# Kernel tuning notes

Measured on AMD Instinct MI355X. Metric: run time of the kernel, lower is better.

The kernel has to match this reference:

```python
import jax, jax.numpy as jnp
import numpy as np

N, E = 2048, 6144
DV_IN, DV_OUT = 128, 64
DE_IN, DE_OUT = 16, 16


def setup_inputs() -> dict:
    key = jax.random.key(0)
    ks = jax.random.split(key, 11)
    return {
        "H_v": jax.random.normal(ks[0], (N, DV_IN), jnp.float32),
        "H_e": jax.random.normal(ks[1], (E, DE_IN), jnp.float32),
        "adj_v": jax.random.uniform(ks[2], (N, N), jnp.float32),
        "adj_e": jax.random.uniform(ks[3], (E, E), jnp.float32),
        "T": jax.random.normal(ks[4], (N, E), jnp.float32),
        "W_v": jax.random.normal(ks[5], (DV_IN, DV_OUT), jnp.float32) * (1.0 / np.sqrt(DV_OUT)),
        "b_v": jax.random.normal(ks[6], (DV_OUT,), jnp.float32) * 0.01,
        "p_v": jax.random.normal(ks[7], (1, DE_IN), jnp.float32),
        "W_e": jax.random.normal(ks[8], (DE_IN, DE_OUT), jnp.float32) * (1.0 / np.sqrt(DE_OUT)),
        "b_e": jax.random.normal(ks[9], (DE_OUT,), jnp.float32) * 0.01,
        "p_e": jax.random.normal(ks[10], (1, DV_OUT), jnp.float32),
    }


def reference(H_v, H_e, adj_v, adj_e, T, W_v, b_v, p_v, W_e, b_e, p_e):
    n, e = T.shape
    # ---- node layer (AlternateConvolution, node_layer=True) ----
    d_e = (H_e @ p_v.T)[:, 0]                      # [E] per-edge diag values
    mult1 = (T * d_e[None, :]) @ T.T               # T @ diag(d_e) @ T^T -> [N,N]
    idx_n = jnp.arange(n)
    M1 = mult1.at[idx_n, idx_n].set(1.0)           # eye*1 + (1-eye)*multiplier
    adjusted_Av = M1 * adj_v
    Hv_out = adjusted_Av @ (H_v @ W_v) + b_v       # [N, DV_OUT]
    # ---- edge layer (AlternateConvolution, node_layer=False) ----
    d_v = (Hv_out @ p_e.T)[:, 0]                   # [N] per-node diag values
    mult2 = (T.T * d_v[None, :]) @ T               # T^T @ diag(d_v) @ T -> [E,E]
    idx_e = jnp.arange(e)
    M2 = mult2.at[idx_e, idx_e].set(1.0)
    adjusted_Ae = M2 * adj_e
    norm_Ae = adjusted_Ae / (adjusted_Ae.max(axis=0, keepdims=True) + 1e-10)
    He_out = norm_Ae @ (H_e @ W_e) + b_e           # [E, DE_OUT]
    return Hv_out, He_out
```

## Files before the change

### kernel.cpp

```cpp
#include <hip/hip_runtime.h>

typedef unsigned short u16;
typedef unsigned int u32;
typedef __bf16 bf16x8 __attribute__((ext_vector_type(8)));
typedef float f32x4 __attribute__((ext_vector_type(4)));

#define NN 2048
#define NE 6144
#define DVIN 128
#define DVOUT 64
#define DEIN 16
#define DEOUT 16

__device__ __forceinline__ u16 f2b(float f) {
  __bf16 b = (__bf16)f;
  return __builtin_bit_cast(u16, b);
}

__device__ __forceinline__ void async16(const void* g, void* l) {
  __builtin_amdgcn_global_load_lds(
      (const __attribute__((address_space(1))) void*)g,
      (__attribute__((address_space(3))) void*)l, 16, 0, 0);
}

__device__ __forceinline__ bf16x8 load8(const u16* p) {
  union { uint4 u; bf16x8 b; } w;
  w.u = *(const uint4*)p;
  return w.b;
}


__global__ __launch_bounds__(256) void k_de(const float* __restrict__ He,
                                            const float* __restrict__ pv,
                                            float* __restrict__ de) {
  int j = blockIdx.x * 256 + threadIdx.x;
  float s = 0.f;
#pragma unroll
  for (int k = 0; k < DEIN; k++) s += He[j * DEIN + k] * pv[k];
  de[j] = s;
}

__global__ __launch_bounds__(256) void k_tb(const float* __restrict__ T,
                                            const float* __restrict__ de,
                                            u16* __restrict__ Tb,
                                            u16* __restrict__ Tbs) {
  size_t idx = (size_t)blockIdx.x * 256 + threadIdx.x;
  size_t f = idx * 8;
  float4 v0 = *(const float4*)(T + f);
  float4 v1 = *(const float4*)(T + f + 4);
  int col = (int)(f % (size_t)NE);
  float4 d0 = *(const float4*)(de + col);
  float4 d1 = *(const float4*)(de + col + 4);
  float v[8] = {v0.x, v0.y, v0.z, v0.w, v1.x, v1.y, v1.z, v1.w};
  float d[8] = {d0.x, d0.y, d0.z, d0.w, d1.x, d1.y, d1.z, d1.w};
  union { u16 s[8]; uint4 u; } a, b;
#pragma unroll
  for (int j = 0; j < 8; j++) { a.s[j] = f2b(v[j]); b.s[j] = f2b(v[j] * d[j]); }
  *(uint4*)(Tb + f) = a.u;
  *(uint4*)(Tbs + f) = b.u;
}

__global__ __launch_bounds__(256) void k_x(const float* __restrict__ Hv,
                                           const float* __restrict__ Wv,
                                           u16* __restrict__ Xt) {
  int i = blockIdx.x * 256 + threadIdx.x;
  int d = blockIdx.y;
  float s = 0.f;
#pragma unroll 8
  for (int k = 0; k < DVIN; k++) s += Hv[i * DVIN + k] * Wv[k * DVOUT + d];
  Xt[(size_t)d * NN + i] = f2b(s);
}

__global__ __launch_bounds__(256) void k_dv(const float* __restrict__ HvOut,
                                            const float* __restrict__ pe,
                                            float* __restrict__ dv) {
  int i = blockIdx.x * 256 + threadIdx.x;
  float s = 0.f;
#pragma unroll
  for (int c = 0; c < DVOUT; c++) s += HvOut[i * DVOUT + c] * pe[c];
  dv[i] = s;
}

__global__ __launch_bounds__(256) void k_tt(const float* __restrict__ T,
                                            const float* __restrict__ dv,
                                            u16* __restrict__ Tt,
                                            u16* __restrict__ Tts) {
  __shared__ float tile[32][33];
  int tx = threadIdx.x, ty = threadIdx.y;
  int bx = blockIdx.x, by = blockIdx.y;
  int col = bx * 32 + tx;
#pragma unroll
  for (int r = 0; r < 4; r++) {
    int row = by * 32 + ty + r * 8;
    tile[ty + r * 8][tx] = T[(size_t)row * NE + col];
  }
  __syncthreads();
  int ocol = by * 32 + tx;
  float dvv = dv[ocol];
#pragma unroll
  for (int r = 0; r < 4; r++) {
    int orow = bx * 32 + ty + r * 8;
    float v = tile[tx][ty + r * 8];
    Tt[(size_t)orow * NN + ocol] = f2b(v);
    Tts[(size_t)orow * NN + ocol] = f2b(v * dvv);
  }
}

__global__ __launch_bounds__(256) void k_zt(const float* __restrict__ He,
                                            const float* __restrict__ We,
                                            const u32* __restrict__ colmax,
                                            u16* __restrict__ Ztb) {
  int b = blockIdx.x * 256 + threadIdx.x;
  float h[16];
  const float4* hp = (const float4*)(He + (size_t)b * DEIN);
#pragma unroll
  for (int q = 0; q < 4; q++) {
    float4 t = hp[q];
    h[q * 4 + 0] = t.x; h[q * 4 + 1] = t.y; h[q * 4 + 2] = t.z; h[q * 4 + 3] = t.w;
  }
  float inv = 1.0f / (__uint_as_float(colmax[b]) + 1e-10f);
#pragma unroll
  for (int d = 0; d < DEOUT; d++) {
    float s = 0.f;
#pragma unroll
    for (int k = 0; k < DEIN; k++) s += h[k] * We[k * DEOUT + d];
    Ztb[(size_t)d * NE + b] = f2b(s * inv);
  }
}

#define BM 128
#define BN 128
#define BK 64

template <int EPI>
__global__ __launch_bounds__(256) void gemm_bt(const u16* __restrict__ A,
                                               const u16* __restrict__ B,
                                               const float* __restrict__ adj,
                                               u16* __restrict__ C,
                                               u32* __restrict__ colmax,
                                               int M, int N, int K) {
  __shared__ u16 As[BM * BK];
  __shared__ u16 Bs[BN * BK];
  __shared__ u32 cmaxLds[BN];

  const int t = threadIdx.x;
  const int bm0 = blockIdx.y * BM, bn0 = blockIdx.x * BN;
  const int wave = t >> 6, lane = t & 63;
  const int lr = lane & 15, kg = lane >> 4;
  const int wm = (wave >> 1) * 64, wn = (wave & 1) * 64;

  if (EPI == 2 && t < BN) cmaxLds[t] = 0u;

  f32x4 acc[4][4];
#pragma unroll
  for (int i = 0; i < 4; i++)
#pragma unroll
    for (int j = 0; j < 4; j++) acc[i][j] = (f32x4){0.f, 0.f, 0.f, 0.f};

  const int arow = t >> 3;
  const int acolsw = (((t & 7) ^ (arow & 7)) * 8);
  const u16* Ag = A + (size_t)(bm0 + arow) * K + acolsw;
  const u16* Bg = B + (size_t)(bn0 + arow) * K + acolsw;
  u16* Al = &As[t * 8];
  u16* Bl = &Bs[t * 8];

  for (int k0 = 0; k0 < K; k0 += BK) {
    __syncthreads();
#pragma unroll
    for (int r = 0; r < 4; r++) {
      async16(Ag + (size_t)(r * 32) * K + k0, Al + r * 32 * BK);
      async16(Bg + (size_t)(r * 32) * K + k0, Bl + r * 32 * BK);
    }
    __syncthreads();
#pragma unroll
    for (int kk = 0; kk < BK; kk += 32) {
      bf16x8 af[4], bf[4];
#pragma unroll
      for (int mi = 0; mi < 4; mi++) {
        int row = wm + mi * 16 + lr;
        int c = (kk >> 3) + kg;
        af[mi] = load8(&As[row * BK + ((c ^ (row & 7)) << 3)]);
      }
#pragma unroll
      for (int ni = 0; ni < 4; ni++) {
        int row = wn + ni * 16 + lr;
        int c = (kk >> 3) + kg;
        bf[ni] = load8(&Bs[row * BK + ((c ^ (row & 7)) << 3)]);
      }
#pragma unroll
      for (int mi = 0; mi < 4; mi++)
#pragma unroll
        for (int ni = 0; ni < 4; ni++)
          acc[mi][ni] = __builtin_amdgcn_mfma_f32_16x16x32_bf16(
              af[mi], bf[ni], acc[mi][ni], 0, 0, 0);
    }
  }

#pragma unroll
  for (int ni = 0; ni < 4; ni++) {
    const int cj = bn0 + wn + ni * 16 + lr;
    float cm = 0.f;
#pragma unroll
    for (int mi = 0; mi < 4; mi++) {
#pragma unroll
      for (int r = 0; r < 4; r++) {
        const int ci = bm0 + wm + mi * 16 + kg * 4 + r;
        float v = acc[mi][ni][r];
        if (ci == cj) v = 1.0f;
        v *= adj[(size_t)ci * N + cj];
        C[(size_t)ci * N + cj] = f2b(v);
        if (EPI == 2) cm = fmaxf(cm, v);
      }
    }
    if (EPI == 2)
      atomicMax(&cmaxLds[wn + ni * 16 + lr], __float_as_uint(cm));
  }
  if (EPI == 2) {
    __syncthreads();
    if (t < BN) atomicMax(&colmax[bn0 + t], cmaxLds[t]);
  }
}


__global__ __launch_bounds__(256) void k_hv(const u16* __restrict__ A1,
                                            const u16* __restrict__ Xt,
                                            const float* __restrict__ bv,
                                            float* __restrict__ out) {
  __shared__ float red[4 * 1024];
  const int t = threadIdx.x, wave = t >> 6, lane = t & 63;
  const int lr = lane & 15, kg = lane >> 4;
  const int m0 = blockIdx.x * 16;
  const int K = NN;
  f32x4 acc[4];
#pragma unroll
  for (int i = 0; i < 4; i++) acc[i] = (f32x4){0.f, 0.f, 0.f, 0.f};
  const int kbeg = wave * (K / 4), kend = kbeg + (K / 4);
  for (int k = kbeg; k < kend; k += 32) {
    bf16x8 af = load8(&A1[(size_t)(m0 + lr) * K + k + kg * 8]);
#pragma unroll
    for (int ni = 0; ni < 4; ni++) {
      bf16x8 bfr = load8(&Xt[(size_t)(ni * 16 + lr) * K + k + kg * 8]);
      acc[ni] = __builtin_amdgcn_mfma_f32_16x16x32_bf16(af, bfr, acc[ni], 0, 0, 0);
    }
  }
#pragma unroll
  for (int ni = 0; ni < 4; ni++)
#pragma unroll
    for (int r = 0; r < 4; r++)
      red[wave * 1024 + (kg * 4 + r) * 64 + ni * 16 + lr] = acc[ni][r];
  __syncthreads();
#pragma unroll
  for (int q = 0; q < 4; q++) {
    int e = t + 256 * q;
    int row = e >> 6, col = e & 63;
    float v = red[e] + red[1024 + e] + red[2048 + e] + red[3072 + e] + bv[col];
    out[(size_t)(m0 + row) * DVOUT + col] = v;
  }
}

__global__ __launch_bounds__(256) void k_he(const u16* __restrict__ adjE,
                                            const u16* __restrict__ Ztb,
                                            const float* __restrict__ be,
                                            float* __restrict__ out) {
  __shared__ float red[4 * 256];
  const int t = threadIdx.x, wave = t >> 6, lane = t & 63;
  const int lr = lane & 15, kg = lane >> 4;
  const int m0 = blockIdx.x * 16;
  const int K = NE;
  f32x4 acc = (f32x4){0.f, 0.f, 0.f, 0.f};
  const int kbeg = wave * (K / 4), kend = kbeg + (K / 4);
  for (int k = kbeg; k < kend; k += 32) {
    bf16x8 af = load8(&adjE[(size_t)(m0 + lr) * K + k + kg * 8]);
    bf16x8 bfr = load8(&Ztb[(size_t)lr * K + k + kg * 8]);
    acc = __builtin_amdgcn_mfma_f32_16x16x32_bf16(af, bfr, acc, 0, 0, 0);
  }
#pragma unroll
  for (int r = 0; r < 4; r++)
    red[wave * 256 + (kg * 4 + r) * 16 + lr] = acc[r];
  __syncthreads();
  {
    int row = t >> 4, col = t & 15;
    float v = red[t] + red[256 + t] + red[512 + t] + red[768 + t] + be[col];
    out[(size_t)(m0 + row) * DEOUT + col] = v;
  }
}

extern "C" void kernel_launch(void* const* d_in, const int* in_sizes, int n_in,
                              void* d_out, int out_size, void* d_ws, size_t ws_size,
                              hipStream_t stream) {
  const float* H_v = (const float*)d_in[0];
  const float* H_e = (const float*)d_in[1];
  const float* adj_v = (const float*)d_in[2];
  const float* adj_e = (const float*)d_in[3];
  const float* T = (const float*)d_in[4];
  const float* W_v = (const float*)d_in[5];
  const float* b_v = (const float*)d_in[6];
  const float* p_v = (const float*)d_in[7];
  const float* W_e = (const float*)d_in[8];
  const float* b_e = (const float*)d_in[9];
  const float* p_e = (const float*)d_in[10];
  float* outHv = (float*)d_out;
  float* outHe = (float*)d_out + NN * DVOUT;

  char* ws = (char*)d_ws;
  u16* Tb   = (u16*)(ws + 0);
  u16* Tbs  = (u16*)(ws + 25165824);
  u16* Tt   = (u16*)(ws + 50331648);
  u16* Tts  = (u16*)(ws + 75497472);
  u16* adjE = (u16*)(ws + 100663296);
  u16* A1   = (u16*)(ws + 176160768);
  u16* Xt   = (u16*)(ws + 184549376);
  u16* Ztb  = (u16*)(ws + 184811520);
  float* de = (float*)(ws + 185008128);
  float* dv = (float*)(ws + 185032704);
  u32* cmax = (u32*)(ws + 185040896);

  k_de<<<NE / 256, 256, 0, stream>>>(H_e, p_v, de);
  k_tb<<<(NN * (size_t)NE) / 8 / 256, 256, 0, stream>>>(T, de, Tb, Tbs);
  k_x<<<dim3(NN / 256, DVOUT), 256, 0, stream>>>(H_v, W_v, Xt);
  gemm_bt<1><<<dim3(NN / BN, NN / BM), 256, 0, stream>>>(
      Tbs, Tb, adj_v, A1, nullptr, NN, NN, NE);
  k_hv<<<NN / 16, 256, 0, stream>>>(A1, Xt, b_v, outHv);
  k_dv<<<NN / 256, 256, 0, stream>>>(outHv, p_e, dv);
  k_tt<<<dim3(NE / 32, NN / 32), dim3(32, 8), 0, stream>>>(T, dv, Tt, Tts);
  hipMemsetAsync(cmax, 0, NE * sizeof(u32), stream);
  gemm_bt<2><<<dim3(NE / BN, NE / BM), 256, 0, stream>>>(
      Tts, Tt, adj_e, adjE, cmax, NE, NE, NN);
  k_zt<<<NE / 256, 256, 0, stream>>>(H_e, W_e, cmax, Ztb);
  k_he<<<NE / 16, 256, 0, stream>>>(adjE, Ztb, b_e, outHe);
}
```

Before: 643.6 us.

## Exploit symmetry of T·diag·Tᵀ products and split-K the node gemm

Both multiplier matrices are symmetric, so the gemms now compute only upper-triangular tiles and mirror the result through LDS into the transposed tile. The edge gemm writes both tiles and updates column maxima for both. The node gemm also adds a 4-way split-K into fp32 partials, summed by a new combine kernel that applies the diagonal and adjacency mask. This roughly halves the MFMA work, at the cost of extra partial-buffer traffic, an extra launch, and idle blocks below the diagonal.

```diff
diff --git a/kernel.cpp b/kernel.cpp
--- a/kernel.cpp
+++ b/kernel.cpp
@@ -12,9 +12,18 @@
 #define DEIN 16
 #define DEOUT 16
 
+#define BM 128
+#define BN 128
+#define BK 64
+#define MS 132
+
 __device__ __forceinline__ u16 f2b(float f) {
   __bf16 b = (__bf16)f;
   return __builtin_bit_cast(u16, b);
+}
+
+__device__ __forceinline__ float b2f(u16 u) {
+  return __uint_as_float(((u32)u) << 16);
 }
 
 __device__ __forceinline__ void async16(const void* g, void* l) {
@@ -128,34 +137,17 @@
   }
 }
 
-#define BM 128
-#define BN 128
-#define BK 64
-
-template <int EPI>
-__global__ __launch_bounds__(256) void gemm_bt(const u16* __restrict__ A,
-                                               const u16* __restrict__ B,
-                                               const float* __restrict__ adj,
-                                               u16* __restrict__ C,
-                                               u32* __restrict__ colmax,
-                                               int M, int N, int K) {
-  __shared__ u16 As[BM * BK];
-  __shared__ u16 Bs[BN * BK];
-  __shared__ u32 cmaxLds[BN];
-
+__device__ __forceinline__ void tile_loop(const u16* __restrict__ A,
+                                          const u16* __restrict__ B,
+                                          int bm0, int bn0, int K,
+                                          int kbeg, int kend,
+                                          u16* As, u16* Bs,
+                                          f32x4 (&acc)[4][4]) {
   const int t = threadIdx.x;
-  const int bm0 = blockIdx.y * BM, bn0 = blockIdx.x * BN;
-  const int wave = t >> 6, lane = t & 63;
+  const int lane = t & 63;
   const int lr = lane & 15, kg = lane >> 4;
+  const int wave = t >> 6;
   const int wm = (wave >> 1) * 64, wn = (wave & 1) * 64;
-
-  if (EPI == 2 && t < BN) cmaxLds[t] = 0u;
-
-  f32x4 acc[4][4];
-#pragma unroll
-  for (int i = 0; i < 4; i++)
-#pragma unroll
-    for (int j = 0; j < 4; j++) acc[i][j] = (f32x4){0.f, 0.f, 0.f, 0.f};
 
   const int arow = t >> 3;
   const int acolsw = (((t & 7) ^ (arow & 7)) * 8);
@@ -164,7 +156,7 @@
   u16* Al = &As[t * 8];
   u16* Bl = &Bs[t * 8];
 
-  for (int k0 = 0; k0 < K; k0 += BK) {
+  for (int k0 = kbeg; k0 < kend; k0 += BK) {
     __syncthreads();
 #pragma unroll
     for (int r = 0; r < 4; r++) {
@@ -195,29 +187,180 @@
               af[mi], bf[ni], acc[mi][ni], 0, 0, 0);
     }
   }
-
+}
+
+__global__ __launch_bounds__(256) void gemm_sym1(const u16* __restrict__ A,
+                                                 const u16* __restrict__ B,
+                                                 float* __restrict__ P) {
+  const int bi = blockIdx.y, bj = blockIdx.x;
+  if (bj < bi) return;
+  __shared__ u16 As[BM * BK];
+  __shared__ u16 Bs[BN * BK];
+  const int bm0 = bi * BM, bn0 = bj * BN;
+  const int K = NE, kc = NE / 4;
+  f32x4 acc[4][4];
+#pragma unroll
+  for (int i = 0; i < 4; i++)
+#pragma unroll
+    for (int j = 0; j < 4; j++) acc[i][j] = (f32x4){0.f, 0.f, 0.f, 0.f};
+
+  tile_loop(A, B, bm0, bn0, K, blockIdx.z * kc, (blockIdx.z + 1) * kc, As, Bs, acc);
+
+  const int t = threadIdx.x, lane = t & 63, lr = lane & 15, kg = lane >> 4;
+  const int wave = t >> 6, wm = (wave >> 1) * 64, wn = (wave & 1) * 64;
+  float* Pz = P + (size_t)blockIdx.z * NN * NN;
 #pragma unroll
   for (int ni = 0; ni < 4; ni++) {
     const int cj = bn0 + wn + ni * 16 + lr;
-    float cm = 0.f;
-#pragma unroll
-    for (int mi = 0; mi < 4; mi++) {
+#pragma unroll
+    for (int mi = 0; mi < 4; mi++)
 #pragma unroll
       for (int r = 0; r < 4; r++) {
         const int ci = bm0 + wm + mi * 16 + kg * 4 + r;
+        Pz[(size_t)ci * NN + cj] = acc[mi][ni][r];
+      }
+  }
+}
+
+__global__ __launch_bounds__(256) void k_comb(const float* __restrict__ P,
+                                              const float* __restrict__ adj,
+                                              u16* __restrict__ A1) {
+  const int bi = blockIdx.y, bj = blockIdx.x;
+  if (bj < bi) return;
+  __shared__ float tile[128][129];
+  const int bm0 = bi * 128, bn0 = bj * 128;
+  const int t = threadIdx.x;
+  const bool diagb = (bi == bj);
+  const size_t NP = (size_t)NN * NN;
+  for (int e = t; e < 128 * 32; e += 256) {
+    int row = e >> 5, c4 = (e & 31) * 4;
+    size_t off = (size_t)(bm0 + row) * NN + bn0 + c4;
+    float4 s0 = *(const float4*)(P + off);
+    float4 s1 = *(const float4*)(P + NP + off);
+    float4 s2 = *(const float4*)(P + 2 * NP + off);
+    float4 s3 = *(const float4*)(P + 3 * NP + off);
+    float sv[4] = {s0.x + s1.x + s2.x + s3.x, s0.y + s1.y + s2.y + s3.y,
+                   s0.z + s1.z + s2.z + s3.z, s0.w + s1.w + s2.w + s3.w};
+    if (diagb) {
+#pragma unroll
+      for (int q = 0; q < 4; q++)
+        if (c4 + q == row) sv[q] = 1.0f;
+    }
+    float4 av = *(const float4*)(adj + off);
+    float avv[4] = {av.x, av.y, av.z, av.w};
+    union { u16 h[4]; uint2 u; } o;
+#pragma unroll
+    for (int q = 0; q < 4; q++) {
+      tile[row][c4 + q] = sv[q];
+      o.h[q] = f2b(sv[q] * avv[q]);
+    }
+    *(uint2*)(A1 + off) = o.u;
+  }
+  if (!diagb) {
+    __syncthreads();
+    for (int e = t; e < 128 * 32; e += 256) {
+      int row = e >> 5, c4 = (e & 31) * 4;
+      size_t off = (size_t)(bn0 + row) * NN + bm0 + c4;
+      float4 av = *(const float4*)(adj + off);
+      float avv[4] = {av.x, av.y, av.z, av.w};
+      union { u16 h[4]; uint2 u; } o;
+#pragma unroll
+      for (int q = 0; q < 4; q++) o.h[q] = f2b(tile[c4 + q][row] * avv[q]);
+      *(uint2*)(A1 + off) = o.u;
+    }
+  }
+}
+
+__global__ __launch_bounds__(256) void gemm_sym2(const u16* __restrict__ A,
+                                                 const u16* __restrict__ B,
+                                                 const float* __restrict__ adj,
+                                                 u16* __restrict__ C,
+                                                 u32* __restrict__ colmax) {
+  const int bi = blockIdx.y, bj = blockIdx.x;
+  if (bj < bi) return;
+  __shared__ union {
+    struct { u16 As[BM * BK]; u16 Bs[BN * BK]; } s;
+    u16 mir[128 * MS];
+  } sh;
+  __shared__ u32 cmaxN[128];
+  __shared__ u32 cmaxM[128];
+  const int bm0 = bi * BM, bn0 = bj * BN;
+  const int t = threadIdx.x;
+  const int N = NE, K = NN;
+  const bool diagb = (bi == bj);
+  if (t < 128) { cmaxN[t] = 0u; cmaxM[t] = 0u; }
+
+  f32x4 acc[4][4];
+#pragma unroll
+  for (int i = 0; i < 4; i++)
+#pragma unroll
+    for (int j = 0; j < 4; j++) acc[i][j] = (f32x4){0.f, 0.f, 0.f, 0.f};
+
+  tile_loop(A, B, bm0, bn0, K, 0, K, sh.s.As, sh.s.Bs, acc);
+
+  const int lane = t & 63, lr = lane & 15, kg = lane >> 4;
+  const int wave = t >> 6, wm = (wave >> 1) * 64, wn = (wave & 1) * 64;
+
+  __syncthreads();
+
+#pragma unroll
+  for (int ni = 0; ni < 4; ni++) {
+    const int cjl = wn + ni * 16 + lr;
+    const int cj = bn0 + cjl;
+    float cm = 0.f;
+#pragma unroll
+    for (int mi = 0; mi < 4; mi++) {
+#pragma unroll
+      for (int r = 0; r < 4; r++) {
+        const int cil = wm + mi * 16 + kg * 4 + r;
+        const int ci = bm0 + cil;
         float v = acc[mi][ni][r];
         if (ci == cj) v = 1.0f;
-        v *= adj[(size_t)ci * N + cj];
-        C[(size_t)ci * N + cj] = f2b(v);
-        if (EPI == 2) cm = fmaxf(cm, v);
+        float w = v * adj[(size_t)ci * N + cj];
+        C[(size_t)ci * N + cj] = f2b(w);
+        cm = fmaxf(cm, w);
+        if (!diagb) sh.mir[cjl * MS + cil] = f2b(v);
       }
     }
-    if (EPI == 2)
-      atomicMax(&cmaxLds[wn + ni * 16 + lr], __float_as_uint(cm));
-  }
-  if (EPI == 2) {
+    atomicMax(&cmaxN[cjl], __float_as_uint(cm));
+  }
+
+  if (!diagb) {
     __syncthreads();
-    if (t < BN) atomicMax(&colmax[bn0 + t], cmaxLds[t]);
+    const int rb = t >> 4, cb = (t & 15) * 8;
+    float rmax[8];
+#pragma unroll
+    for (int q = 0; q < 8; q++) rmax[q] = 0.f;
+#pragma unroll
+    for (int rr = 0; rr < 8; rr++) {
+      const int row = rb + rr * 16;
+      union { uint2 u; u16 s[4]; } w0, w1;
+      w0.u = *(const uint2*)&sh.mir[row * MS + cb];
+      w1.u = *(const uint2*)&sh.mir[row * MS + cb + 4];
+      float f[8] = {b2f(w0.s[0]), b2f(w0.s[1]), b2f(w0.s[2]), b2f(w0.s[3]),
+                    b2f(w1.s[0]), b2f(w1.s[1]), b2f(w1.s[2]), b2f(w1.s[3])};
+      const float* ap = adj + (size_t)(bn0 + row) * N + bm0 + cb;
+      float4 a0 = *(const float4*)ap;
+      float4 a1 = *(const float4*)(ap + 4);
+      float a[8] = {a0.x, a0.y, a0.z, a0.w, a1.x, a1.y, a1.z, a1.w};
+      union { u16 s[8]; uint4 u; } o;
+#pragma unroll
+      for (int q = 0; q < 8; q++) {
+        float w = f[q] * a[q];
+        rmax[q] = fmaxf(rmax[q], w);
+        o.s[q] = f2b(w);
+      }
+      *(uint4*)&C[(size_t)(bn0 + row) * N + bm0 + cb] = o.u;
+    }
+#pragma unroll
+    for (int q = 0; q < 8; q++)
+      atomicMax(&cmaxM[cb + q], __float_as_uint(rmax[q]));
+  }
+
+  __syncthreads();
+  if (t < 128) {
+    atomicMax(&colmax[bn0 + t], cmaxN[t]);
+    if (!diagb) atomicMax(&colmax[bm0 + t], cmaxM[t]);
   }
 }
 
@@ -314,18 +457,18 @@
   float* de = (float*)(ws + 185008128);
   float* dv = (float*)(ws + 185032704);
   u32* cmax = (u32*)(ws + 185040896);
+  float* P = (float*)(ws + 50331648);
 
   k_de<<<NE / 256, 256, 0, stream>>>(H_e, p_v, de);
   k_tb<<<(NN * (size_t)NE) / 8 / 256, 256, 0, stream>>>(T, de, Tb, Tbs);
   k_x<<<dim3(NN / 256, DVOUT), 256, 0, stream>>>(H_v, W_v, Xt);
-  gemm_bt<1><<<dim3(NN / BN, NN / BM), 256, 0, stream>>>(
-      Tbs, Tb, adj_v, A1, nullptr, NN, NN, NE);
+  gemm_sym1<<<dim3(NN / BN, NN / BM, 4), 256, 0, stream>>>(Tbs, Tb, P);
+  k_comb<<<dim3(NN / 128, NN / 128), 256, 0, stream>>>(P, adj_v, A1);
   k_hv<<<NN / 16, 256, 0, stream>>>(A1, Xt, b_v, outHv);
   k_dv<<<NN / 256, 256, 0, stream>>>(outHv, p_e, dv);
   k_tt<<<dim3(NE / 32, NN / 32), dim3(32, 8), 0, stream>>>(T, dv, Tt, Tts);
   hipMemsetAsync(cmax, 0, NE * sizeof(u32), stream);
-  gemm_bt<2><<<dim3(NE / BN, NE / BM), 256, 0, stream>>>(
-      Tts, Tt, adj_e, adjE, cmax, NE, NE, NN);
+  gemm_sym2<<<dim3(NE / BN, NE / BM), 256, 0, stream>>>(Tts, Tt, adj_e, adjE, cmax);
   k_zt<<<NE / 256, 256, 0, stream>>>(H_e, W_e, cmax, Ztb);
   k_he<<<NE / 16, 256, 0, stream>>>(adjE, Ztb, b_e, outHe);
 }
```

New measurement: 660.1 us. 2.6% more time.
